# Kernel tuning notes

Measured on AMD Instinct MI355X. Metric: run time of the kernel, lower is better.

Reference implementation:

```python
import jax, jax.numpy as jnp
import numpy as np

D_IN = 1024
D_OUT = 1024
NUM_HEADS = 16
HEAD_DIM = D_OUT // NUM_HEADS


def setup_inputs() -> dict:
    key = jax.random.key(0)
    ks = jax.random.split(key, 6)
    s = 1.0 / np.sqrt(D_IN)
    x = jax.random.normal(ks[0], (2, 2048, D_IN), dtype=jnp.float32)
    Wq = jax.random.uniform(ks[1], (D_IN, D_OUT), jnp.float32, -s, s)
    Wk = jax.random.uniform(ks[2], (D_IN, D_OUT), jnp.float32, -s, s)
    Wv = jax.random.uniform(ks[3], (D_IN, D_OUT), jnp.float32, -s, s)
    Wo = jax.random.uniform(ks[4], (D_OUT, D_OUT), jnp.float32, -s, s)
    bo = jax.random.uniform(ks[5], (D_OUT,), jnp.float32, -s, s)
    return {"x": x, "Wq": Wq, "Wk": Wk, "Wv": Wv, "Wo": Wo, "bo": bo}


def reference(x, Wq, Wk, Wv, Wo, bo):
    b, T, _ = x.shape
    # projections -> [b, heads, T, head_dim]
    def split_heads(y):
        return y.reshape(b, T, NUM_HEADS, HEAD_DIM).transpose(0, 2, 1, 3)
    q = split_heads(x @ Wq)
    k = split_heads(x @ Wk)
    v = split_heads(x @ Wv)
    scores = jnp.einsum("bhqd,bhkd->bhqk", q, k)  # [b,h,T,T]
    causal = jnp.triu(jnp.ones((T, T), dtype=bool), k=1)
    scores = jnp.where(causal, -jnp.inf, scores)
    weights = jax.nn.softmax(scores / np.sqrt(HEAD_DIM), axis=-1)
    # dropout p=0.0 (eval) -> identity
    ctx = jnp.einsum("bhqk,bhkd->bhqd", weights, v)
    ctx = ctx.transpose(0, 2, 1, 3).reshape(b, T, D_OUT)
    return ctx @ Wo + bo
```

## Files before the change

### kernel.cpp

```cpp
#include <hip/hip_runtime.h>
#include <hip/hip_bf16.h>
#include <math.h>

using f32x4  = __attribute__((ext_vector_type(4)))  float;
using f32x16 = __attribute__((ext_vector_type(16))) float;
using s16x8  = __attribute__((ext_vector_type(8)))  short;
using s16x4  = __attribute__((ext_vector_type(4)))  short;
using u32x2  = __attribute__((ext_vector_type(2)))  unsigned;

#define HD 64
#define NH 16
#define TT 2048
#define DIN 1024
#define NB 2
#define M_TOK (NB*TT)
#define PADK 40
#define PSTR2 68

__device__ __forceinline__ ushort f2b(float f) {
  union { float f; unsigned u; } v; v.f = f;
  unsigned u = v.u;
  return (ushort)((u + 0x7FFFu + ((u >> 16) & 1u)) >> 16);
}

__device__ __forceinline__ unsigned cvt_pk_bf16(float lo, float hi) {
  unsigned r;
  asm("v_cvt_pk_bf16_f32 %0, %1, %2" : "=v"(r) : "v"(lo), "v"(hi));
  return r;
}

__device__ __forceinline__ float xhalf_max(float v) {
  u32x2 r = __builtin_amdgcn_permlane32_swap(__float_as_uint(v), __float_as_uint(v), false, false);
  return fmaxf(__uint_as_float(r.x), __uint_as_float(r.y));
}
__device__ __forceinline__ float xhalf_sum(float v) {
  u32x2 r = __builtin_amdgcn_permlane32_swap(__float_as_uint(v), __float_as_uint(v), false, false);
  return __uint_as_float(r.x) + __uint_as_float(r.y);
}

__global__ __launch_bounds__(256) void cvt_f32_bf16(const float* __restrict__ in,
                                                    ushort* __restrict__ out, int n8) {
  int i = blockIdx.x * 256 + threadIdx.x;
  if (i >= n8) return;
  const f32x4* p = (const f32x4*)(in + (size_t)i * 8);
  f32x4 a = p[0], b = p[1];
  s16x8 o;
  o[0]=(short)f2b(a[0]); o[1]=(short)f2b(a[1]); o[2]=(short)f2b(a[2]); o[3]=(short)f2b(a[3]);
  o[4]=(short)f2b(b[0]); o[5]=(short)f2b(b[1]); o[6]=(short)f2b(b[2]); o[7]=(short)f2b(b[3]);
  *(s16x8*)(out + (size_t)i * 8) = o;
}

__global__ __launch_bounds__(256) void transpose_cvt(const float* __restrict__ W,
                                                     ushort* __restrict__ Wt, int K, int N) {
  __shared__ float tile[32][33];
  int nb = blockIdx.x * 32, kb = blockIdx.y * 32;
  int tx = threadIdx.x & 31, ty = threadIdx.x >> 5;
  #pragma unroll
  for (int j = ty; j < 32; j += 8) tile[j][tx] = W[(size_t)(kb + j) * N + nb + tx];
  __syncthreads();
  #pragma unroll
  for (int j = ty; j < 32; j += 8) Wt[(size_t)(nb + j) * K + kb + tx] = f2b(tile[tx][j]);
}

__global__ __launch_bounds__(256) void gemm_qkv(const ushort* __restrict__ Xb,
                                                const ushort* __restrict__ Wt,
                                                ushort* __restrict__ Qb,
                                                ushort* __restrict__ Kb,
                                                ushort* __restrict__ Vt) {
  __shared__ ushort Al[128 * PADK];
  __shared__ ushort Bl[128 * PADK];
  int tid = threadIdx.x, lane = tid & 63, wid = tid >> 6;
  int wr = wid >> 1, wc = wid & 1, g = lane >> 4, c = lane & 15;
  int m0 = blockIdx.y * 128, n0 = blockIdx.x * 128;
  f32x4 acc[4][4] = {};
  for (int k0 = 0; k0 < DIN; k0 += 32) {
    __syncthreads();
    #pragma unroll
    for (int j = 0; j < 2; ++j) {
      int ci = tid + j * 256;
      int row = ci >> 2, part = ci & 3;
      *(s16x8*)&Al[row * PADK + part * 8] =
          *(const s16x8*)&Xb[(size_t)(m0 + row) * DIN + k0 + part * 8];
      *(s16x8*)&Bl[row * PADK + part * 8] =
          *(const s16x8*)&Wt[(size_t)(n0 + row) * DIN + k0 + part * 8];
    }
    __syncthreads();
    s16x8 af[4], bfr[4];
    #pragma unroll
    for (int i = 0; i < 4; ++i) {
      af[i]  = *(const s16x8*)&Al[(wr * 64 + i * 16 + c) * PADK + g * 8];
      bfr[i] = *(const s16x8*)&Bl[(wc * 64 + i * 16 + c) * PADK + g * 8];
    }
    #pragma unroll
    for (int i = 0; i < 4; ++i)
      #pragma unroll
      for (int jn = 0; jn < 4; ++jn)
        acc[i][jn] = __builtin_amdgcn_mfma_f32_16x16x32_bf16(af[i], bfr[jn], acc[i][jn], 0, 0, 0);
  }
  #pragma unroll
  for (int i = 0; i < 4; ++i)
    #pragma unroll
    for (int jn = 0; jn < 4; ++jn) {
      int mrow = m0 + wr * 64 + i * 16 + g * 4;
      int n = n0 + wc * 64 + jn * 16 + c;
      int b = mrow >> 11, t = mrow & (TT - 1);
      int which = n >> 10, nn = n & 1023, h = nn >> 6, d = nn & 63;
      size_t bh = (size_t)(b * NH + h);
      if (which == 2) {
        s16x4 pk;
        pk[0]=(short)f2b(acc[i][jn][0]); pk[1]=(short)f2b(acc[i][jn][1]);
        pk[2]=(short)f2b(acc[i][jn][2]); pk[3]=(short)f2b(acc[i][jn][3]);
        *(s16x4*)&Vt[(bh * HD + d) * TT + t] = pk;
      } else {
        float sc = (which == 0) ? 0.125f * 1.44269504f : 1.0f;
        ushort* dst = (which == 0) ? &Qb[(bh * TT + t) * HD + d]
                                   : &Kb[(bh * TT + t) * HD + d];
        #pragma unroll
        for (int r = 0; r < 4; ++r) dst[(size_t)r * HD] = f2b(acc[i][jn][r] * sc);
      }
    }
}

__global__ __launch_bounds__(256, 2) void attn_fwd(const ushort* __restrict__ Qb,
                                                   const ushort* __restrict__ Kb,
                                                   const ushort* __restrict__ Vt,
                                                   ushort* __restrict__ Ctx) {
  __shared__ __align__(16) char smem[17920];
  int L = blockIdx.x;
  int xcd = L & 7, j = L >> 3;
  int bh = xcd + 8 * (j & 3);
  int qc = 63 - (j >> 2);
  int q0 = qc * 32;
  const ushort* Qh = Qb + (size_t)bh * TT * HD;
  const ushort* Kh = Kb + (size_t)bh * TT * HD;
  const ushort* Vh = Vt + (size_t)bh * HD * TT;
  int tid = threadIdx.x, lane = tid & 63, w = tid >> 6;
  int hi = lane >> 5, c32 = lane & 31;
  int q_abs = q0 + c32;
  int nt64 = (q0 + 32 + 63) >> 6;

  ushort* pw = (ushort*)smem + w * (32 * PSTR2);

  s16x8 qf[4];
  #pragma unroll
  for (int s = 0; s < 4; ++s)
    qf[s] = *(const s16x8*)&Qh[(size_t)q_abs * HD + s * 16 + 8 * hi];

  f32x16 cA[2] = {};
  float m = -INFINITY, l = 0.f;

  s16x8 kfc[8];
  {
    int tt = (w < nt64) ? w : 0;
    #pragma unroll
    for (int ss = 0; ss < 2; ++ss)
      #pragma unroll
      for (int s = 0; s < 4; ++s)
        kfc[ss * 4 + s] =
            *(const s16x8*)&Kh[(size_t)(tt * 64 + ss * 32 + c32) * HD + s * 16 + 8 * hi];
  }

  for (int t = w; t < nt64; t += 4) {
    int kv0 = t * 64;
    s16x8 vf[2][4];
    #pragma unroll
    for (int dt = 0; dt < 2; ++dt)
      #pragma unroll
      for (int ks = 0; ks < 4; ++ks)
        vf[dt][ks] = *(const s16x8*)&Vh[(size_t)(dt * 32 + c32) * TT + kv0 + ks * 16 + 8 * hi];
    f32x16 S0 = {}, S1 = {};
    #pragma unroll
    for (int s = 0; s < 4; ++s)
      S0 = __builtin_amdgcn_mfma_f32_32x32x16_bf16(kfc[s], qf[s], S0, 0, 0, 0);
    #pragma unroll
    for (int s = 0; s < 4; ++s)
      S1 = __builtin_amdgcn_mfma_f32_32x32x16_bf16(kfc[4 + s], qf[s], S1, 0, 0, 0);
    if (t + 4 < nt64) {
      #pragma unroll
      for (int ss = 0; ss < 2; ++ss)
        #pragma unroll
        for (int s = 0; s < 4; ++s)
          kfc[ss * 4 + s] =
              *(const s16x8*)&Kh[(size_t)((t + 4) * 64 + ss * 32 + c32) * HD + s * 16 + 8 * hi];
    }
    if (kv0 + 63 > q0) {
      #pragma unroll
      for (int r = 0; r < 16; ++r) {
        int base = kv0 + (r & 3) + 8 * (r >> 2) + 4 * hi;
        S0[r] = (base > q_abs) ? -INFINITY : S0[r];
        S1[r] = (base + 32 > q_abs) ? -INFINITY : S1[r];
      }
    }
    float mx[8];
    #pragma unroll
    for (int i = 0; i < 8; ++i)
      mx[i] = fmaxf(fmaxf(S0[2 * i], S0[2 * i + 1]), fmaxf(S1[2 * i], S1[2 * i + 1]));
    #pragma unroll
    for (int i = 0; i < 4; ++i) mx[i] = fmaxf(mx[i], mx[i + 4]);
    mx[0] = fmaxf(fmaxf(mx[0], mx[2]), fmaxf(mx[1], mx[3]));
    float tmax = xhalf_max(mx[0]);
    if (__any(tmax > m + 8.f)) {
      float mnew = fmaxf(m, tmax);
      float alpha = exp2f(m - mnew);
      l *= alpha;
      #pragma unroll
      for (int dt = 0; dt < 2; ++dt)
        #pragma unroll
        for (int r = 0; r < 16; ++r) cA[dt][r] *= alpha;
      m = mnew;
    }
    #pragma unroll
    for (int r = 0; r < 16; ++r) { S0[r] = exp2f(S0[r] - m); S1[r] = exp2f(S1[r] - m); }
    float sm[8];
    #pragma unroll
    for (int i = 0; i < 8; ++i)
      sm[i] = (S0[2 * i] + S0[2 * i + 1]) + (S1[2 * i] + S1[2 * i + 1]);
    #pragma unroll
    for (int i = 0; i < 4; ++i) sm[i] += sm[i + 4];
    float rsum = (sm[0] + sm[2]) + (sm[1] + sm[3]);
    l += xhalf_sum(rsum);
    #pragma unroll
    for (int jj = 0; jj < 8; ++jj) {
      int kvb = ((2 * jj) & 3) + 8 * (jj >> 1) + 4 * hi;
      *(unsigned*)&pw[c32 * PSTR2 + kvb]      = cvt_pk_bf16(S0[2 * jj], S0[2 * jj + 1]);
      *(unsigned*)&pw[c32 * PSTR2 + 32 + kvb] = cvt_pk_bf16(S1[2 * jj], S1[2 * jj + 1]);
    }
    asm volatile("s_waitcnt lgkmcnt(0)" ::: "memory");
    #pragma unroll
    for (int ks = 0; ks < 4; ++ks) {
      s16x8 pf = *(const s16x8*)&pw[c32 * PSTR2 + ks * 16 + 8 * hi];
      cA[0] = __builtin_amdgcn_mfma_f32_32x32x16_bf16(vf[0][ks], pf, cA[0], 0, 0, 0);
      cA[1] = __builtin_amdgcn_mfma_f32_32x32x16_bf16(vf[1][ks], pf, cA[1], 0, 0, 0);
    }
  }

  __syncthreads();
  float* cb = (float*)smem;
  float* mb = (float*)(smem + 10240);
  float* lb = mb + 128;
  if (!hi) { mb[w * 32 + c32] = m; lb[w * 32 + c32] = l; }
  __syncthreads();

  int q  = tid >> 3;
  int dp = (tid & 7) * 2;
  float ew[4];
  {
    float mw[4];
    #pragma unroll
    for (int ww = 0; ww < 4; ++ww) mw[ww] = mb[ww * 32 + q];
    float mG = fmaxf(fmaxf(mw[0], mw[1]), fmaxf(mw[2], mw[3]));
    float lt = 0.f;
    #pragma unroll
    for (int ww = 0; ww < 4; ++ww) {
      ew[ww] = exp2f(mw[ww] - mG);
      lt += ew[ww] * lb[ww * 32 + q];
    }
    float inv = 1.f / lt;
    #pragma unroll
    for (int ww = 0; ww < 4; ++ww) ew[ww] *= inv;
  }
  int b = bh >> 4, h = bh & 15;
  #pragma unroll
  for (int rd = 0; rd < 4; ++rd) {
    int dt = rd >> 1, rh = rd & 1;
    float* dstq = &cb[(size_t)(w * 32 + c32) * 20];
    f32x4 v0 = { cA[dt][rh * 8 + 0], cA[dt][rh * 8 + 1], cA[dt][rh * 8 + 2], cA[dt][rh * 8 + 3] };
    f32x4 v1 = { cA[dt][rh * 8 + 4], cA[dt][rh * 8 + 5], cA[dt][rh * 8 + 6], cA[dt][rh * 8 + 7] };
    *(f32x4*)&dstq[4 * hi]     = v0;
    *(f32x4*)&dstq[8 + 4 * hi] = v1;
    __syncthreads();
    float s0 = 0.f, s1 = 0.f;
    #pragma unroll
    for (int ww = 0; ww < 4; ++ww) {
      const float* src = &cb[(size_t)(ww * 32 + q) * 20 + dp];
      s0 += ew[ww] * src[0];
      s1 += ew[ww] * src[1];
    }
    int dcol = h * HD + 32 * dt + 16 * rh + dp;
    *(unsigned*)&Ctx[((size_t)(b * TT) + q0 + q) * DIN + dcol] = cvt_pk_bf16(s0, s1);
    if (rd < 3) __syncthreads();
  }
}

__global__ __launch_bounds__(256) void gemm_out(const ushort* __restrict__ Cb,
                                                const ushort* __restrict__ Wot,
                                                const float* __restrict__ bo,
                                                float* __restrict__ Out) {
  __shared__ ushort Al[128 * PADK];
  __shared__ ushort Bl[128 * PADK];
  int tid = threadIdx.x, lane = tid & 63, wid = tid >> 6;
  int wr = wid >> 1, wc = wid & 1, g = lane >> 4, c = lane & 15;
  int m0 = blockIdx.y * 128, n0 = blockIdx.x * 128;
  f32x4 acc[4][4] = {};
  for (int k0 = 0; k0 < DIN; k0 += 32) {
    __syncthreads();
    #pragma unroll
    for (int j = 0; j < 2; ++j) {
      int ci = tid + j * 256;
      int row = ci >> 2, part = ci & 3;
      *(s16x8*)&Al[row * PADK + part * 8] =
          *(const s16x8*)&Cb[(size_t)(m0 + row) * DIN + k0 + part * 8];
      *(s16x8*)&Bl[row * PADK + part * 8] =
          *(const s16x8*)&Wot[(size_t)(n0 + row) * DIN + k0 + part * 8];
    }
    __syncthreads();
    s16x8 af[4], bfr[4];
    #pragma unroll
    for (int i = 0; i < 4; ++i) {
      af[i]  = *(const s16x8*)&Al[(wr * 64 + i * 16 + c) * PADK + g * 8];
      bfr[i] = *(const s16x8*)&Bl[(wc * 64 + i * 16 + c) * PADK + g * 8];
    }
    #pragma unroll
    for (int i = 0; i < 4; ++i)
      #pragma unroll
      for (int jn = 0; jn < 4; ++jn)
        acc[i][jn] = __builtin_amdgcn_mfma_f32_16x16x32_bf16(af[i], bfr[jn], acc[i][jn], 0, 0, 0);
  }
  #pragma unroll
  for (int i = 0; i < 4; ++i)
    #pragma unroll
    for (int jn = 0; jn < 4; ++jn) {
      int mrow = m0 + wr * 64 + i * 16 + g * 4;
      int n = n0 + wc * 64 + jn * 16 + c;
      float bias = bo[n];
      float* dst = &Out[(size_t)mrow * DIN + n];
      #pragma unroll
      for (int r = 0; r < 4; ++r) dst[(size_t)r * DIN] = acc[i][jn][r] + bias;
    }
}

extern "C" void kernel_launch(void* const* d_in, const int* in_sizes, int n_in,
                              void* d_out, int out_size, void* d_ws, size_t ws_size,
                              hipStream_t stream) {
  const float* x  = (const float*)d_in[0];
  const float* Wq = (const float*)d_in[1];
  const float* Wk = (const float*)d_in[2];
  const float* Wv = (const float*)d_in[3];
  const float* Wo = (const float*)d_in[4];
  const float* bo = (const float*)d_in[5];
  float* Out = (float*)d_out;

  char* ws = (char*)d_ws;
  size_t off = 0;
  auto alloc = [&](size_t bytes) -> char* {
    char* p = ws + off;
    off += (bytes + 255) & ~(size_t)255;
    return p;
  };
  ushort* Xb  = (ushort*)alloc((size_t)M_TOK * DIN * 2);
  ushort* Wt3 = (ushort*)alloc((size_t)3 * 1024 * DIN * 2);
  ushort* Wot = (ushort*)alloc((size_t)1024 * 1024 * 2);
  ushort* Qb  = (ushort*)alloc((size_t)NB * NH * TT * HD * 2);
  ushort* Kb  = (ushort*)alloc((size_t)NB * NH * TT * HD * 2);
  ushort* Vt  = (ushort*)alloc((size_t)NB * NH * TT * HD * 2);
  ushort* Cb  = (ushort*)alloc((size_t)M_TOK * DIN * 2);

  cvt_f32_bf16<<<(M_TOK * DIN / 8 + 255) / 256, 256, 0, stream>>>(x, Xb, M_TOK * DIN / 8);
  dim3 tgrid(1024 / 32, 1024 / 32);
  transpose_cvt<<<tgrid, 256, 0, stream>>>(Wq, Wt3,                   1024, 1024);
  transpose_cvt<<<tgrid, 256, 0, stream>>>(Wk, Wt3 + 1024 * 1024,     1024, 1024);
  transpose_cvt<<<tgrid, 256, 0, stream>>>(Wv, Wt3 + 2 * 1024 * 1024, 1024, 1024);
  transpose_cvt<<<tgrid, 256, 0, stream>>>(Wo, Wot,                   1024, 1024);

  gemm_qkv<<<dim3(3072 / 128, M_TOK / 128), 256, 0, stream>>>(Xb, Wt3, Qb, Kb, Vt);
  attn_fwd<<<2048, 256, 0, stream>>>(Qb, Kb, Vt, Cb);
  gemm_out<<<dim3(1024 / 128, M_TOK / 128), 256, 0, stream>>>(Cb, Wot, bo, Out);
}
```

Before: 238.5 us.

## Load GEMM tiles via global_load_lds and merge weight transposes into one launch

Both projection GEMMs now stage A and B tiles with direct global-to-LDS loads (global_load_lds, 16 bytes per lane) instead of loading through registers and then storing to LDS. The padded LDS stride is dropped to an unpadded 32-element layout, as the direct-load path requires. The four weight transpose/convert kernels are merged into one launch using blockIdx.z. This removes register round-trips and VALU work during tile staging and cuts launch overhead, but the unpadded layout may bring LDS bank conflicts on the fragment reads.

```diff
diff --git a/kernel.cpp b/kernel.cpp
--- a/kernel.cpp
+++ b/kernel.cpp
@@ -14,7 +14,6 @@
 #define DIN 1024
 #define NB 2
 #define M_TOK (NB*TT)
-#define PADK 40
 #define PSTR2 68
 
 __device__ __forceinline__ ushort f2b(float f) {
@@ -36,6 +35,12 @@
 __device__ __forceinline__ float xhalf_sum(float v) {
   u32x2 r = __builtin_amdgcn_permlane32_swap(__float_as_uint(v), __float_as_uint(v), false, false);
   return __uint_as_float(r.x) + __uint_as_float(r.y);
+}
+
+__device__ __forceinline__ void gll16(const ushort* g, ushort* l) {
+  __builtin_amdgcn_global_load_lds(
+      (const __attribute__((address_space(1))) unsigned*)g,
+      (__attribute__((address_space(3))) unsigned*)l, 16, 0, 0);
 }
 
 __global__ __launch_bounds__(256) void cvt_f32_bf16(const float* __restrict__ in,
@@ -50,16 +55,23 @@
   *(s16x8*)(out + (size_t)i * 8) = o;
 }
 
-__global__ __launch_bounds__(256) void transpose_cvt(const float* __restrict__ W,
-                                                     ushort* __restrict__ Wt, int K, int N) {
+__global__ __launch_bounds__(256) void transpose_cvt4(const float* __restrict__ W0,
+                                                      const float* __restrict__ W1,
+                                                      const float* __restrict__ W2,
+                                                      const float* __restrict__ W3,
+                                                      ushort* __restrict__ Wt3,
+                                                      ushort* __restrict__ Wot) {
   __shared__ float tile[32][33];
+  int z = blockIdx.z;
+  const float* W = (z == 0) ? W0 : (z == 1) ? W1 : (z == 2) ? W2 : W3;
+  ushort* Wt = (z < 3) ? (Wt3 + (size_t)z * 1024 * 1024) : Wot;
   int nb = blockIdx.x * 32, kb = blockIdx.y * 32;
   int tx = threadIdx.x & 31, ty = threadIdx.x >> 5;
   #pragma unroll
-  for (int j = ty; j < 32; j += 8) tile[j][tx] = W[(size_t)(kb + j) * N + nb + tx];
+  for (int j = ty; j < 32; j += 8) tile[j][tx] = W[(size_t)(kb + j) * 1024 + nb + tx];
   __syncthreads();
   #pragma unroll
-  for (int j = ty; j < 32; j += 8) Wt[(size_t)(nb + j) * K + kb + tx] = f2b(tile[tx][j]);
+  for (int j = ty; j < 32; j += 8) Wt[(size_t)(nb + j) * 1024 + kb + tx] = f2b(tile[tx][j]);
 }
 
 __global__ __launch_bounds__(256) void gemm_qkv(const ushort* __restrict__ Xb,
@@ -67,29 +79,28 @@
                                                 ushort* __restrict__ Qb,
                                                 ushort* __restrict__ Kb,
                                                 ushort* __restrict__ Vt) {
-  __shared__ ushort Al[128 * PADK];
-  __shared__ ushort Bl[128 * PADK];
-  int tid = threadIdx.x, lane = tid & 63, wid = tid >> 6;
+  __shared__ ushort Al[128 * 32];
+  __shared__ ushort Bl[128 * 32];
+  int tid = threadIdx.x, lane = tid & 63;
+  int wid = tid >> 6;
   int wr = wid >> 1, wc = wid & 1, g = lane >> 4, c = lane & 15;
   int m0 = blockIdx.y * 128, n0 = blockIdx.x * 128;
+  int row1 = tid >> 2, part = tid & 3;
+  int row2 = 64 + row1;
+  int wbase = (tid & ~63) * 8;
   f32x4 acc[4][4] = {};
   for (int k0 = 0; k0 < DIN; k0 += 32) {
     __syncthreads();
-    #pragma unroll
-    for (int j = 0; j < 2; ++j) {
-      int ci = tid + j * 256;
-      int row = ci >> 2, part = ci & 3;
-      *(s16x8*)&Al[row * PADK + part * 8] =
-          *(const s16x8*)&Xb[(size_t)(m0 + row) * DIN + k0 + part * 8];
-      *(s16x8*)&Bl[row * PADK + part * 8] =
-          *(const s16x8*)&Wt[(size_t)(n0 + row) * DIN + k0 + part * 8];
-    }
+    gll16(&Xb[(size_t)(m0 + row1) * DIN + k0 + part * 8], &Al[wbase]);
+    gll16(&Xb[(size_t)(m0 + row2) * DIN + k0 + part * 8], &Al[2048 + wbase]);
+    gll16(&Wt[(size_t)(n0 + row1) * DIN + k0 + part * 8], &Bl[wbase]);
+    gll16(&Wt[(size_t)(n0 + row2) * DIN + k0 + part * 8], &Bl[2048 + wbase]);
     __syncthreads();
     s16x8 af[4], bfr[4];
     #pragma unroll
     for (int i = 0; i < 4; ++i) {
-      af[i]  = *(const s16x8*)&Al[(wr * 64 + i * 16 + c) * PADK + g * 8];
-      bfr[i] = *(const s16x8*)&Bl[(wc * 64 + i * 16 + c) * PADK + g * 8];
+      af[i]  = *(const s16x8*)&Al[(wr * 64 + i * 16 + c) * 32 + g * 8];
+      bfr[i] = *(const s16x8*)&Bl[(wc * 64 + i * 16 + c) * 32 + g * 8];
     }
     #pragma unroll
     for (int i = 0; i < 4; ++i)
@@ -286,29 +297,28 @@
                                                 const ushort* __restrict__ Wot,
                                                 const float* __restrict__ bo,
                                                 float* __restrict__ Out) {
-  __shared__ ushort Al[128 * PADK];
-  __shared__ ushort Bl[128 * PADK];
-  int tid = threadIdx.x, lane = tid & 63, wid = tid >> 6;
+  __shared__ ushort Al[128 * 32];
+  __shared__ ushort Bl[128 * 32];
+  int tid = threadIdx.x, lane = tid & 63;
+  int wid = tid >> 6;
   int wr = wid >> 1, wc = wid & 1, g = lane >> 4, c = lane & 15;
   int m0 = blockIdx.y * 128, n0 = blockIdx.x * 128;
+  int row1 = tid >> 2, part = tid & 3;
+  int row2 = 64 + row1;
+  int wbase = (tid & ~63) * 8;
   f32x4 acc[4][4] = {};
   for (int k0 = 0; k0 < DIN; k0 += 32) {
     __syncthreads();
-    #pragma unroll
-    for (int j = 0; j < 2; ++j) {
-      int ci = tid + j * 256;
-      int row = ci >> 2, part = ci & 3;
-      *(s16x8*)&Al[row * PADK + part * 8] =
-          *(const s16x8*)&Cb[(size_t)(m0 + row) * DIN + k0 + part * 8];
-      *(s16x8*)&Bl[row * PADK + part * 8] =
-          *(const s16x8*)&Wot[(size_t)(n0 + row) * DIN + k0 + part * 8];
-    }
+    gll16(&Cb[(size_t)(m0 + row1) * DIN + k0 + part * 8], &Al[wbase]);
+    gll16(&Cb[(size_t)(m0 + row2) * DIN + k0 + part * 8], &Al[2048 + wbase]);
+    gll16(&Wot[(size_t)(n0 + row1) * DIN + k0 + part * 8], &Bl[wbase]);
+    gll16(&Wot[(size_t)(n0 + row2) * DIN + k0 + part * 8], &Bl[2048 + wbase]);
     __syncthreads();
     s16x8 af[4], bfr[4];
     #pragma unroll
     for (int i = 0; i < 4; ++i) {
-      af[i]  = *(const s16x8*)&Al[(wr * 64 + i * 16 + c) * PADK + g * 8];
-      bfr[i] = *(const s16x8*)&Bl[(wc * 64 + i * 16 + c) * PADK + g * 8];
+      af[i]  = *(const s16x8*)&Al[(wr * 64 + i * 16 + c) * 32 + g * 8];
+      bfr[i] = *(const s16x8*)&Bl[(wc * 64 + i * 16 + c) * 32 + g * 8];
     }
     #pragma unroll
     for (int i = 0; i < 4; ++i)
@@ -356,11 +366,7 @@
   ushort* Cb  = (ushort*)alloc((size_t)M_TOK * DIN * 2);
 
   cvt_f32_bf16<<<(M_TOK * DIN / 8 + 255) / 256, 256, 0, stream>>>(x, Xb, M_TOK * DIN / 8);
-  dim3 tgrid(1024 / 32, 1024 / 32);
-  transpose_cvt<<<tgrid, 256, 0, stream>>>(Wq, Wt3,                   1024, 1024);
-  transpose_cvt<<<tgrid, 256, 0, stream>>>(Wk, Wt3 + 1024 * 1024,     1024, 1024);
-  transpose_cvt<<<tgrid, 256, 0, stream>>>(Wv, Wt3 + 2 * 1024 * 1024, 1024, 1024);
-  transpose_cvt<<<tgrid, 256, 0, stream>>>(Wo, Wot,                   1024, 1024);
+  transpose_cvt4<<<dim3(32, 32, 4), 256, 0, stream>>>(Wq, Wk, Wv, Wo, Wt3, Wot);
 
   gemm_qkv<<<dim3(3072 / 128, M_TOK / 128), 256, 0, stream>>>(Xb, Wt3, Qb, Kb, Vt);
   attn_fwd<<<2048, 256, 0, stream>>>(Qb, Kb, Vt, Cb);
```

New measurement: 227.6 us. -4.6%, faster.
